# Optimization experiments

Measured on AMD Instinct MI355X. Metric: run time of the kernel, lower is better.

The kernel has to match this reference:

```python
import jax, jax.numpy as jnp
import numpy as np

B, S, E, H = 2, 2048, 1024, 16
D = E // H  # head_dim = 64


def setup_inputs() -> dict:
    key = jax.random.key(0)
    ks = jax.random.split(key, 8)
    s = 0.02
    return {
        "queries": jax.random.normal(ks[0], (B, S, E), jnp.float32),
        "keys": jax.random.normal(ks[1], (B, S, E), jnp.float32),
        "values": jax.random.normal(ks[2], (B, S, E), jnp.float32),
        "mask": jnp.ones((B, 1, 1, S), jnp.int32),
        "Wq": jax.random.normal(ks[3], (E, E), jnp.float32) * s,
        "bq": jnp.zeros((E,), jnp.float32),
        "Wk": jax.random.normal(ks[4], (E, E), jnp.float32) * s,
        "bk": jnp.zeros((E,), jnp.float32),
        "Wv": jax.random.normal(ks[5], (E, E), jnp.float32) * s,
        "bv": jnp.zeros((E,), jnp.float32),
        "Wo": jax.random.normal(ks[6], (E, E), jnp.float32) * s,
        "bo": jnp.zeros((E,), jnp.float32),
    }


def reference(queries, keys, values, mask, Wq, bq, Wk, bk, Wv, bv, Wo, bo):
    # NOTE: faithful to source, W_v is applied to the `keys` input; `values` is unused.
    q = queries @ Wq.T + bq            # [B,S,E]
    k = keys @ Wk.T + bk               # [B,S,E]
    v = keys @ Wv.T + bv               # [B,S,E]
    q = q.reshape(B, S, H, D)
    k = k.reshape(B, S, H, D)
    v = v.reshape(B, S, H, D)
    scale = 1.0 / jnp.sqrt(jnp.asarray(D, q.dtype))
    scores = jnp.einsum("nqhd,nkhd->nhqk", q, k)   # [B,H,S,S] full score matrix
    scores = jnp.where(mask == 0, jnp.asarray(-1e20, scores.dtype), scores)
    attn = jax.nn.softmax(scores * scale, axis=-1)
    out = jnp.einsum("nhqk,nkhd->nqhd", attn, v).reshape(B, S, E)
    return out @ Wo.T + bo
```

## Files before the change

### kernel.cpp

```cpp
#include <hip/hip_runtime.h>
#include <hip/hip_bf16.h>
#include <stdint.h>

#define NB 2
#define NS 2048
#define NE 1024
#define NH 16
#define ND 64
#define NT 32

typedef __attribute__((ext_vector_type(4))) float f32x4;
typedef __attribute__((ext_vector_type(16))) float f32x16;
typedef __attribute__((ext_vector_type(8))) short s16x8;
typedef __attribute__((ext_vector_type(4))) unsigned short u16x4;
typedef __attribute__((ext_vector_type(2))) unsigned int uint2v;

__device__ __forceinline__ unsigned short f2bf(float f) {
  union { float f; unsigned int i; } u; u.f = f;
  unsigned int r = u.i + 0x7FFFu + ((u.i >> 16) & 1u);
  return (unsigned short)(r >> 16);
}

__device__ __forceinline__ unsigned cvtpk_bf16(float lo, float hi) {
  unsigned r;
  asm("v_cvt_pk_bf16_f32 %0, %1, %2" : "=v"(r) : "v"(lo), "v"(hi));
  return r;
}

__device__ __forceinline__ void gload_lds16(const void* g, void* l) {
  __builtin_amdgcn_global_load_lds(
      (const __attribute__((address_space(1))) uint32_t*)g,
      (__attribute__((address_space(3))) uint32_t*)l, 16, 0, 0);
}

__device__ __forceinline__ f32x4 mfma16(s16x8 a, s16x8 b, f32x4 c) {
  return __builtin_amdgcn_mfma_f32_16x16x32_bf16(a, b, c, 0, 0, 0);
}
__device__ __forceinline__ f32x16 mfma32(s16x8 a, s16x8 b, f32x16 c) {
  return __builtin_amdgcn_mfma_f32_32x32x16_bf16(a, b, c, 0, 0, 0);
}

__global__ void prep(const float* __restrict__ xq, const float* __restrict__ xk,
                     unsigned short* __restrict__ dq, unsigned short* __restrict__ dk,
                     const float* __restrict__ w0, const float* __restrict__ w1,
                     const float* __restrict__ w2, const float* __restrict__ w3,
                     unsigned short* __restrict__ e0, unsigned short* __restrict__ e1,
                     unsigned short* __restrict__ e2, unsigned short* __restrict__ e3,
                     const int* __restrict__ mask, unsigned long long* __restrict__ bm) {
  const int bid = blockIdx.x, t = threadIdx.x;
  if (bid < 2048) {
    const float* s = (bid < 1024) ? xq : xk;
    unsigned short* d = (bid < 1024) ? dq : dk;
    int i = (bid & 1023) * 256 + t;
    const int n4 = NB * NS * NE / 4, stride = 1024 * 256;
    for (; i < n4; i += stride) {
      float4 v = ((const float4*)s)[i];
      u16x4 o;
      o.x = f2bf(v.x); o.y = f2bf(v.y); o.z = f2bf(v.z); o.w = f2bf(v.w);
      ((u16x4*)d)[i] = o;
    }
  } else if (bid < 3072) {
    int seg = (bid - 2048) >> 8;
    const float* s; unsigned short* d;
    switch (seg) {
      case 0: s = w0; d = e0; break;
      case 1: s = w1; d = e1; break;
      case 2: s = w2; d = e2; break;
      default: s = w3; d = e3; break;
    }
    int i = ((bid - 2048) & 255) * 256 + t;
    const int n4 = NE * NE / 4, stride = 256 * 256;
    for (; i < n4; i += stride) {
      float4 v = ((const float4*)s)[i];
      u16x4 o;
      o.x = f2bf(v.x); o.y = f2bf(v.y); o.z = f2bf(v.z); o.w = f2bf(v.w);
      ((u16x4*)d)[i] = o;
    }
  } else {
    int w = (bid - 3072) * 4 + (t >> 6);
    int lane = t & 63;
    int mk = mask[w * 64 + lane];
    unsigned long long bal = __ballot(mk != 0);
    if (lane == 0) bm[w] = bal;
  }
}

__global__ __launch_bounds__(256, 3) void gemm_qkv(
    const unsigned short* __restrict__ Aq, const unsigned short* __restrict__ Akv,
    const unsigned short* __restrict__ Wqp, const unsigned short* __restrict__ Wkp,
    const unsigned short* __restrict__ Wvp,
    const float* __restrict__ bqp, const float* __restrict__ bkp, const float* __restrict__ bvp,
    unsigned short* __restrict__ outq, unsigned short* __restrict__ outk,
    unsigned short* __restrict__ outvt) {
  constexpr int BM = 64, K = 1024;
  __shared__ char smem[2 * (BM * 128 + 16384)];
  const int t = threadIdx.x;
  const int lane = t & 63;
  const int wv = t >> 6;
  const int wr = wv >> 1, wc = wv & 1;
  const int x = blockIdx.x;
  const int bm = blockIdx.y * BM;
  const int lr = lane & 15, lg = lane >> 4;

  const unsigned short* A; const unsigned short* Wp; const float* bp;
  unsigned short* outp; int nloc, mode;
  float qsc;
  if (x < 8)       { A = Aq;  Wp = Wqp; bp = bqp; outp = outq;  nloc = x * 128;        mode = 0; qsc = 0.18033688f; }
  else if (x < 16) { A = Akv; Wp = Wkp; bp = bkp; outp = outk;  nloc = (x - 8) * 128;  mode = 0; qsc = 1.0f; }
  else             { A = Akv; Wp = Wvp; bp = bvp; outp = outvt; nloc = (x - 16) * 128; mode = 1; qsc = 1.0f; }

  f32x4 acc[2][4] = {};

  auto stage = [&](int buf, int k0) {
    char* As = smem + buf * (BM * 128 + 16384);
    char* Bs = As + BM * 128;
#pragma unroll
    for (int r = 0; r < 2; ++r) {
      int lin = r * 256 + t;
      int row = lin >> 3;
      int scb = ((lin & 7) << 4) ^ ((row & 7) << 4);
      gload_lds16((const char*)(A + (size_t)(bm + row) * K + k0) + scb,
                  As + (size_t)(r * 256 + (t & ~63)) * 16);
    }
#pragma unroll
    for (int r = 0; r < 4; ++r) {
      int lin = r * 256 + t;
      int row = lin >> 3;
      int scb = ((lin & 7) << 4) ^ ((row & 7) << 4);
      gload_lds16((const char*)(Wp + (size_t)(nloc + row) * K + k0) + scb,
                  Bs + (size_t)(r * 256 + (t & ~63)) * 16);
    }
  };

  stage(0, 0);
  for (int t6 = 0; t6 < K / 64; ++t6) {
    const int cur = t6 & 1;
    if (t6 + 1 < K / 64) {
      stage(cur ^ 1, (t6 + 1) * 64);
      asm volatile("s_waitcnt vmcnt(6)" ::: "memory");
    } else {
      asm volatile("s_waitcnt vmcnt(0)" ::: "memory");
    }
    asm volatile("s_barrier" ::: "memory");

    const char* As = smem + cur * (BM * 128 + 16384);
    const char* Bs = As + BM * 128;
    s16x8 af[2][2], bfr[4][2];
#pragma unroll
    for (int mf = 0; mf < 2; ++mf)
#pragma unroll
      for (int kk = 0; kk < 2; ++kk) {
        int row = wr * 32 + mf * 16 + lr;
        int cb = (lg << 4) + (kk << 6);
        af[mf][kk] = *(const s16x8*)(As + row * 128 + (cb ^ ((row & 7) << 4)));
      }
#pragma unroll
    for (int nf = 0; nf < 4; ++nf)
#pragma unroll
      for (int kk = 0; kk < 2; ++kk) {
        int row = wc * 64 + nf * 16 + lr;
        int cb = (lg << 4) + (kk << 6);
        bfr[nf][kk] = *(const s16x8*)(Bs + row * 128 + (cb ^ ((row & 7) << 4)));
      }
#pragma unroll
    for (int mf = 0; mf < 2; ++mf)
#pragma unroll
      for (int nf = 0; nf < 4; ++nf)
#pragma unroll
        for (int kk = 0; kk < 2; ++kk)
          acc[mf][nf] = mfma16(af[mf][kk], bfr[nf][kk], acc[mf][nf]);

    asm volatile("s_waitcnt lgkmcnt(0)" ::: "memory");
    asm volatile("s_barrier" ::: "memory");
  }

#pragma unroll
  for (int mf = 0; mf < 2; ++mf)
#pragma unroll
    for (int nf = 0; nf < 4; ++nf) {
      int m0 = bm + wr * 32 + mf * 16 + (lg << 2);
      int nc = wc * 64 + nf * 16 + lr;
      float bv = bp[nloc + nc];
      if (mode == 0) {
#pragma unroll
        for (int r = 0; r < 4; ++r)
          outp[(size_t)(m0 + r) * 1024 + nloc + nc] = f2bf((acc[mf][nf][r] + bv) * qsc);
      } else {
        int b = m0 >> 11, s = m0 & 2047;
        u16x4 o;
        o.x = f2bf(acc[mf][nf][0] + bv);
        o.y = f2bf(acc[mf][nf][1] + bv);
        o.z = f2bf(acc[mf][nf][2] + bv);
        o.w = f2bf(acc[mf][nf][3] + bv);
        *(u16x4*)&outp[((size_t)b * NE + nloc + nc) * NS + s] = o;
      }
    }
}

__global__ __launch_bounds__(256, 3) void gemm_o(
    const unsigned short* __restrict__ A, const unsigned short* __restrict__ W,
    const float* __restrict__ bias, float* __restrict__ out) {
  constexpr int BM = 64, K = 1024;
  __shared__ char smem[2 * (BM * 128 + 16384)];
  const int t = threadIdx.x;
  const int lane = t & 63;
  const int wv = t >> 6;
  const int wr = wv >> 1, wc = wv & 1;
  const int bm = blockIdx.y * BM, bn = blockIdx.x * 128;
  const int lr = lane & 15, lg = lane >> 4;

  f32x4 acc[2][4] = {};

  auto stage = [&](int buf, int k0) {
    char* As = smem + buf * (BM * 128 + 16384);
    char* Bs = As + BM * 128;
#pragma unroll
    for (int r = 0; r < 2; ++r) {
      int lin = r * 256 + t;
      int row = lin >> 3;
      int scb = ((lin & 7) << 4) ^ ((row & 7) << 4);
      gload_lds16((const char*)(A + (size_t)(bm + row) * K + k0) + scb,
                  As + (size_t)(r * 256 + (t & ~63)) * 16);
    }
#pragma unroll
    for (int r = 0; r < 4; ++r) {
      int lin = r * 256 + t;
      int row = lin >> 3;
      int scb = ((lin & 7) << 4) ^ ((row & 7) << 4);
      gload_lds16((const char*)(W + (size_t)(bn + row) * K + k0) + scb,
                  Bs + (size_t)(r * 256 + (t & ~63)) * 16);
    }
  };

  stage(0, 0);
  for (int t6 = 0; t6 < K / 64; ++t6) {
    const int cur = t6 & 1;
    if (t6 + 1 < K / 64) {
      stage(cur ^ 1, (t6 + 1) * 64);
      asm volatile("s_waitcnt vmcnt(6)" ::: "memory");
    } else {
      asm volatile("s_waitcnt vmcnt(0)" ::: "memory");
    }
    asm volatile("s_barrier" ::: "memory");

    const char* As = smem + cur * (BM * 128 + 16384);
    const char* Bs = As + BM * 128;
    s16x8 af[2][2], bfr[4][2];
#pragma unroll
    for (int mf = 0; mf < 2; ++mf)
#pragma unroll
      for (int kk = 0; kk < 2; ++kk) {
        int row = wr * 32 + mf * 16 + lr;
        int cb = (lg << 4) + (kk << 6);
        af[mf][kk] = *(const s16x8*)(As + row * 128 + (cb ^ ((row & 7) << 4)));
      }
#pragma unroll
    for (int nf = 0; nf < 4; ++nf)
#pragma unroll
      for (int kk = 0; kk < 2; ++kk) {
        int row = wc * 64 + nf * 16 + lr;
        int cb = (lg << 4) + (kk << 6);
        bfr[nf][kk] = *(const s16x8*)(Bs + row * 128 + (cb ^ ((row & 7) << 4)));
      }
#pragma unroll
    for (int mf = 0; mf < 2; ++mf)
#pragma unroll
      for (int nf = 0; nf < 4; ++nf)
#pragma unroll
        for (int kk = 0; kk < 2; ++kk)
          acc[mf][nf] = mfma16(af[mf][kk], bfr[nf][kk], acc[mf][nf]);

    asm volatile("s_waitcnt lgkmcnt(0)" ::: "memory");
    asm volatile("s_barrier" ::: "memory");
  }

#pragma unroll
  for (int mf = 0; mf < 2; ++mf)
#pragma unroll
    for (int nf = 0; nf < 4; ++nf) {
      int m0 = bm + wr * 32 + mf * 16 + (lg << 2);
      int n = bn + wc * 64 + nf * 16 + lr;
      float bv = bias[n];
#pragma unroll
      for (int r = 0; r < 4; ++r)
        out[(size_t)(m0 + r) * 1024 + n] = acc[mf][nf][r] + bv;
    }
}

__global__ __launch_bounds__(512, 2) void attn_fwd(
    const unsigned short* __restrict__ qb, const unsigned short* __restrict__ kb,
    const unsigned short* __restrict__ vt, const unsigned long long* __restrict__ bmw,
    unsigned short* __restrict__ ob) {
  __shared__ char smem[65536];
  const int t = threadIdx.x, lane = t & 63, wv = t >> 6;
  const int l31 = lane & 31, hi = lane >> 5;
  const int sw = (l31 & 15) << 4;
  const int bh = blockIdx.y, b = bh >> 4, h = bh & 15;
  const int q = blockIdx.x * 256 + wv * 32 + l31;

  s16x8 qf[4];
#pragma unroll
  for (int ks = 0; ks < 4; ++ks)
    qf[ks] = *(const s16x8*)&qb[((size_t)(b * NS + q)) * NE + h * ND + ks * 16 + hi * 8];

  unsigned long long mword = bmw[(size_t)b * 32 + l31];
  unsigned mlo = (unsigned)mword, mhi = (unsigned)(mword >> 32);

  const char* kSrc; const char* vSrc; int ldsB;
  {
    int L = t * 16;
    int row = L >> 8;
    int offp = (L & 255) ^ ((row & 15) << 4);
    int rr = row + ((offp >> 7) << 5);
    int byo = offp & 127;
    kSrc = (const char*)&kb[((size_t)(b * NS) + rr) * NE + h * ND] + byo;
    vSrc = (const char*)&vt[((size_t)((b * NH + h) * ND) + rr) * NS] + byo;
    ldsB = (t & ~63) * 16;
  }

  int off16[8];
#pragma unroll
  for (int j = 0; j < 8; ++j)
    off16[j] = l31 * 256 + ((j * 32 + hi * 16) ^ sw);

  auto stage = [&](int buf, int kt) {
    char* base = smem + buf * 16384;
    gload_lds16(kSrc + (size_t)kt * (NE * 2), base + ldsB);
    gload_lds16(vSrc + (size_t)kt * 2, base + 8192 + ldsB);
  };

  f32x16 oacc[2] = {};
  f32x16 lacc = {};
  s16x8 pfp[4];

  auto qk = [&](const char* Ks, f32x16& st0, f32x16& st1) {
#pragma unroll
    for (int ks = 0; ks < 4; ++ks) {
      s16x8 kf = *(const s16x8*)(Ks + off16[ks]);
      st0 = mfma32(kf, qf[ks], st0);
    }
#pragma unroll
    for (int ks = 0; ks < 4; ++ks) {
      s16x8 kf = *(const s16x8*)(Ks + off16[4 + ks]);
      st1 = mfma32(kf, qf[ks], st1);
    }
  };

  auto pv = [&](const char* Vs) {
#pragma unroll
    for (int td = 0; td < 2; ++td)
#pragma unroll
      for (int ks = 0; ks < 4; ++ks) {
        s16x8 vf = *(const s16x8*)(Vs + off16[td * 4 + ks]);
        oacc[td] = mfma32(vf, pfp[ks], oacc[td]);
      }
  };

  auto smpack = [&](int tt, f32x16& st0, f32x16& st1) {
#pragma unroll
    for (int r = 0; r < 16; ++r) st0[r] = __builtin_amdgcn_exp2f(st0[r] - 6.0f);
#pragma unroll
    for (int r = 0; r < 16; ++r) st1[r] = __builtin_amdgcn_exp2f(st1[r] - 6.0f);

    unsigned lo = (unsigned)__builtin_amdgcn_readlane((int)mlo, tt);
    unsigned hh = (unsigned)__builtin_amdgcn_readlane((int)mhi, tt);
    unsigned long long bal = ((unsigned long long)hh << 32) | lo;
    if (bal != ~0ull) {
#pragma unroll
      for (int r = 0; r < 16; ++r) {
        int key0 = (r & 3) + 8 * (r >> 2) + 4 * hi;
        if (!((bal >> key0) & 1)) st0[r] = 0.f;
        if (!((bal >> (key0 + 32)) & 1)) st1[r] = 0.f;
      }
    }

    lacc += st0;
    lacc += st1;

#pragma unroll
    for (int ks = 0; ks < 4; ++ks) {
      const int r0 = (ks & 1) * 8;
      unsigned wreg[4];
#pragma unroll
      for (int w = 0; w < 2; ++w) {
        float e0, e1, e2, e3;
        if (ks < 2) {
          e0 = st0[r0 + 2 * w]; e1 = st0[r0 + 2 * w + 1];
          e2 = st0[r0 + 4 + 2 * w]; e3 = st0[r0 + 4 + 2 * w + 1];
        } else {
          e0 = st1[r0 + 2 * w]; e1 = st1[r0 + 2 * w + 1];
          e2 = st1[r0 + 4 + 2 * w]; e3 = st1[r0 + 4 + 2 * w + 1];
        }
        unsigned x = cvtpk_bf16(e0, e1);
        unsigned y = cvtpk_bf16(e2, e3);
        uint2v r2 = __builtin_amdgcn_permlane32_swap(x, y, false, false);
        wreg[w] = r2.x;
        wreg[w + 2] = r2.y;
      }
      union { unsigned u[4]; s16x8 v; } pu;
      pu.u[0] = wreg[0]; pu.u[1] = wreg[1]; pu.u[2] = wreg[2]; pu.u[3] = wreg[3];
      pfp[ks] = pu.v;
    }
  };

  stage(0, 0);
  stage(1, 64);

  asm volatile("s_waitcnt vmcnt(2)" ::: "memory");
  __builtin_amdgcn_s_barrier();
  stage(2, 128);
  {
    f32x16 s0 = {}, s1 = {};
    __builtin_amdgcn_s_setprio(1);
    qk(smem, s0, s1);
    __builtin_amdgcn_s_setprio(0);
    smpack(0, s0, s1);
  }

#pragma unroll 1
  for (int tt = 1; tt < NT; ++tt) {
    if (tt + 1 < NT) {
      asm volatile("s_waitcnt vmcnt(2)" ::: "memory");
    } else {
      asm volatile("s_waitcnt vmcnt(0)" ::: "memory");
    }
    __builtin_amdgcn_s_barrier();
    if (tt + 2 < NT) stage((tt + 2) & 3, (tt + 2) * 64);

    const char* Kb = smem + (tt & 3) * 16384;
    const char* Vb = smem + ((tt - 1) & 3) * 16384 + 8192;
    f32x16 s0 = {}, s1 = {};
    __builtin_amdgcn_s_setprio(1);
    qk(Kb, s0, s1);
    pv(Vb);
    __builtin_amdgcn_s_setprio(0);
    smpack(tt, s0, s1);
  }

  __builtin_amdgcn_s_setprio(1);
  pv(smem + ((NT - 1) & 3) * 16384 + 8192);
  __builtin_amdgcn_s_setprio(0);

  float l0 = 0.f;
#pragma unroll
  for (int r = 0; r < 16; ++r) l0 += lacc[r];
  float l = l0 + __shfl_xor(l0, 32);
  float inv = 1.0f / l;

  char* Ob = smem + wv * 4096;
#pragma unroll
  for (int td = 0; td < 2; ++td)
#pragma unroll
    for (int i = 0; i < 8; ++i) {
      int r = 2 * i;
      int d = td * 32 + (r & 3) + 8 * (r >> 2) + 4 * hi;
      unsigned pk = cvtpk_bf16(oacc[td][r] * inv, oacc[td][r + 1] * inv);
      *(unsigned*)(Ob + l31 * 128 + ((d * 2) ^ ((l31 & 7) << 4))) = pk;
    }
#pragma unroll
  for (int p4 = 0; p4 < 4; ++p4) {
    int lq = p4 * 8 + (lane >> 3);
    int col = (lane & 7) * 16;
    s16x8 v0 = *(const s16x8*)(Ob + lq * 128 + (col ^ ((lq & 7) << 4)));
    int qg = blockIdx.x * 256 + wv * 32 + lq;
    *(s16x8*)((char*)&ob[((size_t)(b * NS + qg)) * NE + h * ND] + col) = v0;
  }
}

extern "C" void kernel_launch(void* const* d_in, const int* in_sizes, int n_in,
                              void* d_out, int out_size, void* d_ws, size_t ws_size,
                              hipStream_t stream) {
  const float* queries = (const float*)d_in[0];
  const float* keys = (const float*)d_in[1];
  const int* mask = (const int*)d_in[3];
  const float* Wq = (const float*)d_in[4];
  const float* bq = (const float*)d_in[5];
  const float* Wk = (const float*)d_in[6];
  const float* bk = (const float*)d_in[7];
  const float* Wv = (const float*)d_in[8];
  const float* bv = (const float*)d_in[9];
  const float* Wo = (const float*)d_in[10];
  const float* bo = (const float*)d_in[11];
  float* out = (float*)d_out;

  char* ws = (char*)d_ws;
  const size_t SZ_X = (size_t)NB * NS * NE * 2;
  const size_t SZ_W = (size_t)NE * NE * 2;
  unsigned short* qbf = (unsigned short*)(ws);
  unsigned short* kbf = (unsigned short*)(ws + SZ_X);
  unsigned short* wqb = (unsigned short*)(ws + 2 * SZ_X);
  unsigned short* wkb = (unsigned short*)(ws + 2 * SZ_X + SZ_W);
  unsigned short* wvb = (unsigned short*)(ws + 2 * SZ_X + 2 * SZ_W);
  unsigned short* wob = (unsigned short*)(ws + 2 * SZ_X + 3 * SZ_W);
  unsigned short* qp  = (unsigned short*)(ws + 2 * SZ_X + 4 * SZ_W);
  unsigned short* kp  = (unsigned short*)(ws + 3 * SZ_X + 4 * SZ_W);
  unsigned short* vtp = (unsigned short*)(ws + 4 * SZ_X + 4 * SZ_W);
  unsigned short* ao  = (unsigned short*)(ws + 5 * SZ_X + 4 * SZ_W);
  unsigned long long* bmp = (unsigned long long*)(ws + 6 * SZ_X + 4 * SZ_W);

  prep<<<3088, 256, 0, stream>>>(queries, keys, qbf, kbf,
                                 Wq, Wk, Wv, Wo, wqb, wkb, wvb, wob,
                                 mask, bmp);

  gemm_qkv<<<dim3(24, 64), 256, 0, stream>>>(qbf, kbf, wqb, wkb, wvb,
                                             bq, bk, bv, qp, kp, vtp);

  dim3 ga(NS / 256, NB * NH);
  attn_fwd<<<ga, 512, 0, stream>>>(qp, kp, vtp, bmp, ao);

  gemm_o<<<dim3(8, 64), 256, 0, stream>>>(ao, wob, bo, out);
}
```

Before: 108.8 us.

## Use 128x128 tiles with 32x32x16 MFMA for projection GEMMs

Replaces the two 64x128-tile GEMM kernels, which use 16x16x32 MFMA, with a single templated 128x128-tile kernel using 32x32x16 bf16 MFMA and a new 256-byte-row XOR-swizzled LDS layout. Each wave now computes a 64x64 output, which roughly halves the LDS fragment reads per MFMA and lowers global-load traffic per output. In exchange, LDS use grows to 64KB per block, occupancy drops from 3 to 2 blocks, and the grid shrinks to 768 and 256 blocks, which may leave CUs underused for the output projection.

```diff
diff --git a/kernel.cpp b/kernel.cpp
--- a/kernel.cpp
+++ b/kernel.cpp
@@ -33,9 +33,6 @@
       (__attribute__((address_space(3))) uint32_t*)l, 16, 0, 0);
 }
 
-__device__ __forceinline__ f32x4 mfma16(s16x8 a, s16x8 b, f32x4 c) {
-  return __builtin_amdgcn_mfma_f32_16x16x32_bf16(a, b, c, 0, 0, 0);
-}
 __device__ __forceinline__ f32x16 mfma32(s16x8 a, s16x8 b, f32x16 c) {
   return __builtin_amdgcn_mfma_f32_32x32x16_bf16(a, b, c, 0, 0, 0);
 }
@@ -85,205 +82,149 @@
   }
 }
 
-__global__ __launch_bounds__(256, 3) void gemm_qkv(
+
+template <int NX>
+__global__ __launch_bounds__(256, 2) void gemm32(
     const unsigned short* __restrict__ Aq, const unsigned short* __restrict__ Akv,
     const unsigned short* __restrict__ Wqp, const unsigned short* __restrict__ Wkp,
     const unsigned short* __restrict__ Wvp,
     const float* __restrict__ bqp, const float* __restrict__ bkp, const float* __restrict__ bvp,
-    unsigned short* __restrict__ outq, unsigned short* __restrict__ outk,
-    unsigned short* __restrict__ outvt) {
-  constexpr int BM = 64, K = 1024;
-  __shared__ char smem[2 * (BM * 128 + 16384)];
+    void* __restrict__ outq, void* __restrict__ outk, void* __restrict__ outvt) {
+  constexpr int K = 1024;
+  __shared__ char smem[65536];
   const int t = threadIdx.x;
   const int lane = t & 63;
   const int wv = t >> 6;
   const int wr = wv >> 1, wc = wv & 1;
+  const int l31 = lane & 31, hi = lane >> 5;
   const int x = blockIdx.x;
-  const int bm = blockIdx.y * BM;
-  const int lr = lane & 15, lg = lane >> 4;
+  const int bm = blockIdx.y * 128;
 
   const unsigned short* A; const unsigned short* Wp; const float* bp;
-  unsigned short* outp; int nloc, mode;
-  float qsc;
-  if (x < 8)       { A = Aq;  Wp = Wqp; bp = bqp; outp = outq;  nloc = x * 128;        mode = 0; qsc = 0.18033688f; }
-  else if (x < 16) { A = Akv; Wp = Wkp; bp = bkp; outp = outk;  nloc = (x - 8) * 128;  mode = 0; qsc = 1.0f; }
-  else             { A = Akv; Wp = Wvp; bp = bvp; outp = outvt; nloc = (x - 16) * 128; mode = 1; qsc = 1.0f; }
-
-  f32x4 acc[2][4] = {};
+  void* outp; int nloc, mode; float qsc;
+  if (NX == 1) {
+    A = Aq; Wp = Wqp; bp = bqp; outp = outq; nloc = x * 128; mode = 2; qsc = 1.0f;
+  } else if (x < 8) {
+    A = Aq;  Wp = Wqp; bp = bqp; outp = outq;  nloc = x * 128;        mode = 0; qsc = 0.18033688f;
+  } else if (x < 16) {
+    A = Akv; Wp = Wkp; bp = bkp; outp = outk;  nloc = (x - 8) * 128;  mode = 0; qsc = 1.0f;
+  } else {
+    A = Akv; Wp = Wvp; bp = bvp; outp = outvt; nloc = (x - 16) * 128; mode = 1; qsc = 1.0f;
+  }
+
+  int srow[4]; int skby[4];
+#pragma unroll
+  for (int r = 0; r < 4; ++r) {
+    int L = (r * 256 + t) * 16;
+    int row256 = L >> 8;
+    int off = L & 255;
+    int offp = off ^ ((row256 & 15) << 4);
+    srow[r] = row256 + ((offp >> 7) << 6);
+    skby[r] = offp & 127;
+  }
 
   auto stage = [&](int buf, int k0) {
-    char* As = smem + buf * (BM * 128 + 16384);
-    char* Bs = As + BM * 128;
-#pragma unroll
-    for (int r = 0; r < 2; ++r) {
-      int lin = r * 256 + t;
-      int row = lin >> 3;
-      int scb = ((lin & 7) << 4) ^ ((row & 7) << 4);
-      gload_lds16((const char*)(A + (size_t)(bm + row) * K + k0) + scb,
-                  As + (size_t)(r * 256 + (t & ~63)) * 16);
-    }
-#pragma unroll
-    for (int r = 0; r < 4; ++r) {
-      int lin = r * 256 + t;
-      int row = lin >> 3;
-      int scb = ((lin & 7) << 4) ^ ((row & 7) << 4);
-      gload_lds16((const char*)(Wp + (size_t)(nloc + row) * K + k0) + scb,
-                  Bs + (size_t)(r * 256 + (t & ~63)) * 16);
-    }
+    char* As = smem + buf * 32768;
+    char* Bs = As + 16384;
+#pragma unroll
+    for (int r = 0; r < 4; ++r)
+      gload_lds16((const char*)(A + (size_t)(bm + srow[r]) * K + k0) + skby[r],
+                  As + (r * 256 + (t & ~63)) * 16);
+#pragma unroll
+    for (int r = 0; r < 4; ++r)
+      gload_lds16((const char*)(Wp + (size_t)(nloc + srow[r]) * K + k0) + skby[r],
+                  Bs + (r * 256 + (t & ~63)) * 16);
   };
+
+  int abase[2], axor[2], akh[2];
+  int bbase[2], bxor[2], bkh[2];
+#pragma unroll
+  for (int mt = 0; mt < 2; ++mt) {
+    int row = wr * 64 + mt * 32 + l31;
+    abase[mt] = (row & 63) * 256; axor[mt] = (row & 15) << 4; akh[mt] = (row >> 6) * 128;
+    int rowb = wc * 64 + mt * 32 + l31;
+    bbase[mt] = (rowb & 63) * 256; bxor[mt] = (rowb & 15) << 4; bkh[mt] = (rowb >> 6) * 128;
+  }
+
+  f32x16 acc[2][2] = {};
 
   stage(0, 0);
   for (int t6 = 0; t6 < K / 64; ++t6) {
     const int cur = t6 & 1;
     if (t6 + 1 < K / 64) {
       stage(cur ^ 1, (t6 + 1) * 64);
-      asm volatile("s_waitcnt vmcnt(6)" ::: "memory");
+      asm volatile("s_waitcnt vmcnt(8)" ::: "memory");
     } else {
       asm volatile("s_waitcnt vmcnt(0)" ::: "memory");
     }
     asm volatile("s_barrier" ::: "memory");
 
-    const char* As = smem + cur * (BM * 128 + 16384);
-    const char* Bs = As + BM * 128;
-    s16x8 af[2][2], bfr[4][2];
-#pragma unroll
-    for (int mf = 0; mf < 2; ++mf)
-#pragma unroll
-      for (int kk = 0; kk < 2; ++kk) {
-        int row = wr * 32 + mf * 16 + lr;
-        int cb = (lg << 4) + (kk << 6);
-        af[mf][kk] = *(const s16x8*)(As + row * 128 + (cb ^ ((row & 7) << 4)));
-      }
-#pragma unroll
-    for (int nf = 0; nf < 4; ++nf)
-#pragma unroll
-      for (int kk = 0; kk < 2; ++kk) {
-        int row = wc * 64 + nf * 16 + lr;
-        int cb = (lg << 4) + (kk << 6);
-        bfr[nf][kk] = *(const s16x8*)(Bs + row * 128 + (cb ^ ((row & 7) << 4)));
-      }
-#pragma unroll
-    for (int mf = 0; mf < 2; ++mf)
-#pragma unroll
-      for (int nf = 0; nf < 4; ++nf)
-#pragma unroll
-        for (int kk = 0; kk < 2; ++kk)
-          acc[mf][nf] = mfma16(af[mf][kk], bfr[nf][kk], acc[mf][nf]);
+    const char* As = smem + cur * 32768;
+    const char* Bs = As + 16384;
+    s16x8 af[2][4], bf[2][4];
+#pragma unroll
+    for (int mt = 0; mt < 2; ++mt)
+#pragma unroll
+      for (int ks = 0; ks < 4; ++ks)
+        af[mt][ks] = *(const s16x8*)(As + abase[mt] + ((akh[mt] + ks * 32 + hi * 16) ^ axor[mt]));
+#pragma unroll
+    for (int nt = 0; nt < 2; ++nt)
+#pragma unroll
+      for (int ks = 0; ks < 4; ++ks)
+        bf[nt][ks] = *(const s16x8*)(Bs + bbase[nt] + ((bkh[nt] + ks * 32 + hi * 16) ^ bxor[nt]));
+#pragma unroll
+    for (int mt = 0; mt < 2; ++mt)
+#pragma unroll
+      for (int nt = 0; nt < 2; ++nt)
+#pragma unroll
+        for (int ks = 0; ks < 4; ++ks)
+          acc[mt][nt] = mfma32(af[mt][ks], bf[nt][ks], acc[mt][nt]);
 
     asm volatile("s_waitcnt lgkmcnt(0)" ::: "memory");
     asm volatile("s_barrier" ::: "memory");
   }
 
 #pragma unroll
-  for (int mf = 0; mf < 2; ++mf)
-#pragma unroll
-    for (int nf = 0; nf < 4; ++nf) {
-      int m0 = bm + wr * 32 + mf * 16 + (lg << 2);
-      int nc = wc * 64 + nf * 16 + lr;
-      float bv = bp[nloc + nc];
+  for (int mt = 0; mt < 2; ++mt)
+#pragma unroll
+    for (int nt = 0; nt < 2; ++nt) {
+      int m0 = bm + wr * 64 + mt * 32;
+      int n0l = nloc + wc * 64 + nt * 32;
+      float bv = bp[n0l + l31];
       if (mode == 0) {
-#pragma unroll
-        for (int r = 0; r < 4; ++r)
-          outp[(size_t)(m0 + r) * 1024 + nloc + nc] = f2bf((acc[mf][nf][r] + bv) * qsc);
+        unsigned short* C = (unsigned short*)outp;
+#pragma unroll
+        for (int rg = 0; rg < 4; ++rg) {
+          int row = m0 + 4 * hi + 8 * rg;
+#pragma unroll
+          for (int j = 0; j < 4; ++j)
+            C[(size_t)(row + j) * 1024 + n0l + l31] =
+                f2bf((acc[mt][nt][rg * 4 + j] + bv) * qsc);
+        }
+      } else if (mode == 1) {
+        unsigned short* C = (unsigned short*)outp;
+        int b = m0 >> 11;
+        int n = n0l + l31;
+#pragma unroll
+        for (int rg = 0; rg < 4; ++rg) {
+          int s = (m0 + 4 * hi + 8 * rg) & 2047;
+          u16x4 o;
+          o.x = f2bf(acc[mt][nt][rg * 4 + 0] + bv);
+          o.y = f2bf(acc[mt][nt][rg * 4 + 1] + bv);
+          o.z = f2bf(acc[mt][nt][rg * 4 + 2] + bv);
+          o.w = f2bf(acc[mt][nt][rg * 4 + 3] + bv);
+          *(u16x4*)&C[((size_t)b * NE + n) * NS + s] = o;
+        }
       } else {
-        int b = m0 >> 11, s = m0 & 2047;
-        u16x4 o;
-        o.x = f2bf(acc[mf][nf][0] + bv);
-        o.y = f2bf(acc[mf][nf][1] + bv);
-        o.z = f2bf(acc[mf][nf][2] + bv);
-        o.w = f2bf(acc[mf][nf][3] + bv);
-        *(u16x4*)&outp[((size_t)b * NE + nloc + nc) * NS + s] = o;
+        float* C = (float*)outp;
+#pragma unroll
+        for (int rg = 0; rg < 4; ++rg) {
+          int row = m0 + 4 * hi + 8 * rg;
+#pragma unroll
+          for (int j = 0; j < 4; ++j)
+            C[(size_t)(row + j) * 1024 + n0l + l31] = acc[mt][nt][rg * 4 + j] + bv;
+        }
       }
-    }
-}
-
-__global__ __launch_bounds__(256, 3) void gemm_o(
-    const unsigned short* __restrict__ A, const unsigned short* __restrict__ W,
-    const float* __restrict__ bias, float* __restrict__ out) {
-  constexpr int BM = 64, K = 1024;
-  __shared__ char smem[2 * (BM * 128 + 16384)];
-  const int t = threadIdx.x;
-  const int lane = t & 63;
-  const int wv = t >> 6;
-  const int wr = wv >> 1, wc = wv & 1;
-  const int bm = blockIdx.y * BM, bn = blockIdx.x * 128;
-  const int lr = lane & 15, lg = lane >> 4;
-
-  f32x4 acc[2][4] = {};
-
-  auto stage = [&](int buf, int k0) {
-    char* As = smem + buf * (BM * 128 + 16384);
-    char* Bs = As + BM * 128;
-#pragma unroll
-    for (int r = 0; r < 2; ++r) {
-      int lin = r * 256 + t;
-      int row = lin >> 3;
-      int scb = ((lin & 7) << 4) ^ ((row & 7) << 4);
-      gload_lds16((const char*)(A + (size_t)(bm + row) * K + k0) + scb,
-                  As + (size_t)(r * 256 + (t & ~63)) * 16);
-    }
-#pragma unroll
-    for (int r = 0; r < 4; ++r) {
-      int lin = r * 256 + t;
-      int row = lin >> 3;
-      int scb = ((lin & 7) << 4) ^ ((row & 7) << 4);
-      gload_lds16((const char*)(W + (size_t)(bn + row) * K + k0) + scb,
-                  Bs + (size_t)(r * 256 + (t & ~63)) * 16);
-    }
-  };
-
-  stage(0, 0);
-  for (int t6 = 0; t6 < K / 64; ++t6) {
-    const int cur = t6 & 1;
-    if (t6 + 1 < K / 64) {
-      stage(cur ^ 1, (t6 + 1) * 64);
-      asm volatile("s_waitcnt vmcnt(6)" ::: "memory");
-    } else {
-      asm volatile("s_waitcnt vmcnt(0)" ::: "memory");
-    }
-    asm volatile("s_barrier" ::: "memory");
-
-    const char* As = smem + cur * (BM * 128 + 16384);
-    const char* Bs = As + BM * 128;
-    s16x8 af[2][2], bfr[4][2];
-#pragma unroll
-    for (int mf = 0; mf < 2; ++mf)
-#pragma unroll
-      for (int kk = 0; kk < 2; ++kk) {
-        int row = wr * 32 + mf * 16 + lr;
-        int cb = (lg << 4) + (kk << 6);
-        af[mf][kk] = *(const s16x8*)(As + row * 128 + (cb ^ ((row & 7) << 4)));
-      }
-#pragma unroll
-    for (int nf = 0; nf < 4; ++nf)
-#pragma unroll
-      for (int kk = 0; kk < 2; ++kk) {
-        int row = wc * 64 + nf * 16 + lr;
-        int cb = (lg << 4) + (kk << 6);
-        bfr[nf][kk] = *(const s16x8*)(Bs + row * 128 + (cb ^ ((row & 7) << 4)));
-      }
-#pragma unroll
-    for (int mf = 0; mf < 2; ++mf)
-#pragma unroll
-      for (int nf = 0; nf < 4; ++nf)
-#pragma unroll
-        for (int kk = 0; kk < 2; ++kk)
-          acc[mf][nf] = mfma16(af[mf][kk], bfr[nf][kk], acc[mf][nf]);
-
-    asm volatile("s_waitcnt lgkmcnt(0)" ::: "memory");
-    asm volatile("s_barrier" ::: "memory");
-  }
-
-#pragma unroll
-  for (int mf = 0; mf < 2; ++mf)
-#pragma unroll
-    for (int nf = 0; nf < 4; ++nf) {
-      int m0 = bm + wr * 32 + mf * 16 + (lg << 2);
-      int n = bn + wc * 64 + nf * 16 + lr;
-      float bv = bias[n];
-#pragma unroll
-      for (int r = 0; r < 4; ++r)
-        out[(size_t)(m0 + r) * 1024 + n] = acc[mf][nf][r] + bv;
     }
 }
 
@@ -502,11 +443,12 @@
                                  Wq, Wk, Wv, Wo, wqb, wkb, wvb, wob,
                                  mask, bmp);
 
-  gemm_qkv<<<dim3(24, 64), 256, 0, stream>>>(qbf, kbf, wqb, wkb, wvb,
-                                             bq, bk, bv, qp, kp, vtp);
+  gemm32<3><<<dim3(24, 32), 256, 0, stream>>>(qbf, kbf, wqb, wkb, wvb,
+                                              bq, bk, bv, qp, kp, vtp);
 
   dim3 ga(NS / 256, NB * NH);
   attn_fwd<<<ga, 512, 0, stream>>>(qp, kp, vtp, bmp, ao);
 
-  gemm_o<<<dim3(8, 64), 256, 0, stream>>>(ao, wob, bo, out);
-}
+  gemm32<1><<<dim3(8, 32), 256, 0, stream>>>(ao, nullptr, wob, nullptr, nullptr,
+                                             bo, nullptr, nullptr, out, nullptr, nullptr);
+}
```

Measured after the change: 111.3 us. 1.02x slower.
